# Optimization experiments

Hardware: AMD Instinct MI355X
Metric: run time of the kernel (lower is better)

## Reference

```python
import jax, jax.numpy as jnp
import numpy as np

HEADS = 4
F_OUT = 64
NEG_SLOPE = 0.2


def setup_inputs() -> dict:
    key = jax.random.key(0)
    k1, k2, k3, k4 = jax.random.split(key, 4)
    N, F_IN = 4096, 256
    x = jax.random.normal(k1, (N, F_IN), dtype=jnp.float32)
    adj = jax.random.randint(k2, (N, N), 0, 2, dtype=jnp.int32)
    # nn.Linear stores weight [out, in]; we store transposed [in, out] for x @ W
    W = jax.random.normal(k3, (F_IN, F_OUT * HEADS), dtype=jnp.float32) * (1.0 / np.sqrt(F_IN))
    a = jax.random.normal(k4, (2 * F_OUT, 1), dtype=jnp.float32) * 0.1
    return {"x": x, "adj": adj, "W": W, "a": a}


def reference(x, adj, W, a):
    N = x.shape[0]
    h = (x @ W).reshape(N, HEADS, F_OUT)              # [N, H, F]
    # matmul(cat(h_i, h_j), a) == h_i @ a1 + h_j @ a2 (exact, avoids O(N^2*2F) h_cat)
    a1 = a[:F_OUT, 0]
    a2 = a[F_OUT:, 0]
    e_i = jnp.einsum('nhf,f->nh', h, a1)              # [N, H]
    e_j = jnp.einsum('nhf,f->nh', h, a2)              # [N, H]
    e = e_i[:, None, :] + e_j[None, :, :]             # [N, N, H]
    e = jnp.where(e > 0, e, NEG_SLOPE * e)            # LeakyReLU(0.2)
    e = jnp.where(adj[:, :, None] == 0, -jnp.inf, e)
    attention = jax.nn.softmax(e, axis=1)             # softmax over source nodes j
    h_prime = jnp.einsum('ijh,jhf->ihf', attention, h)  # [N, H, F]
    return h_prime.mean(axis=1)                       # heads > 1 -> mean over heads
```

## Files before the change

### kernel.cpp

```cpp
#include <hip/hip_runtime.h>

#define N     4096
#define FIN   256
#define CC    256
#define HEADS 4
#define FOUT  64
#define XPITCH 266

typedef __attribute__((ext_vector_type(8))) short bf16x8;
typedef __attribute__((ext_vector_type(4))) float f32x4;
typedef __attribute__((ext_vector_type(2))) float f32x2;

__device__ inline unsigned cvtpk(float lo, float hi) {
    unsigned r;
    asm("v_cvt_pk_bf16_f32 %0, %1, %2" : "=v"(r) : "v"(lo), "v"(hi));
    return r;
}
__device__ inline f32x2 pkmul(f32x2 a, f32x2 b) {
    f32x2 r;
    asm("v_pk_mul_f32 %0, %1, %2" : "=v"(r) : "v"(a), "v"(b));
    return r;
}

__global__ __launch_bounds__(512) void gat_k1a(const float* __restrict__ x,
                                               const float* __restrict__ W,
                                               const float* __restrict__ a,
                                               short* __restrict__ hF,
                                               float2* __restrict__ e1f,
                                               float2* __restrict__ e2f) {
    __shared__ __align__(16) short xs[64][XPITCH];
    __shared__ __align__(16) short wts[64][XPITCH];
    __shared__ __align__(16) short hbuf[64][74];
    const int t    = threadIdx.x;
    const int bid  = blockIdx.x;
    const int lane = t & 63;
    const int w    = t >> 6;

    const int hd = bid >> 6;
    const int n0 = (bid & 63) * 64;
    const int c0 = hd * 64;

    {
        const float4* xsrc = (const float4*)(x + (size_t)n0 * FIN);
        #pragma unroll
        for (int it = 0; it < 8; ++it) {
            const int fi = it * 512 + t;
            const float4 v = xsrc[fi];
            uint2 o;
            o.x = cvtpk(v.x, v.y);
            o.y = cvtpk(v.z, v.w);
            *(uint2*)&xs[fi >> 6][(fi & 63) * 4] = o;
        }
    }
    {
        const int c  = t & 63;
        const int k4 = (t >> 6) * 4;
        #pragma unroll
        for (int it = 0; it < 8; ++it) {
            const int k = it * 32 + k4;
            const float w0 = W[(k + 0) * CC + c0 + c];
            const float w1 = W[(k + 1) * CC + c0 + c];
            const float w2 = W[(k + 2) * CC + c0 + c];
            const float w3 = W[(k + 3) * CC + c0 + c];
            uint2 o;
            o.x = cvtpk(w0, w1);
            o.y = cvtpk(w2, w3);
            *(uint2*)&wts[c][k] = o;
        }
    }
    __syncthreads();

    const int m = lane & 15;
    const int q = lane >> 4;

    if (w < 4) {
        f32x4 acc[4];
        #pragma unroll
        for (int ct = 0; ct < 4; ++ct) acc[ct] = (f32x4){0.f, 0.f, 0.f, 0.f};

        #pragma unroll
        for (int ks = 0; ks < 8; ++ks) {
            const bf16x8 af = *(const bf16x8*)&xs[w * 16 + m][ks * 32 + q * 8];
            #pragma unroll
            for (int ct = 0; ct < 4; ++ct) {
                const bf16x8 bf_ = *(const bf16x8*)&wts[ct * 16 + m][ks * 32 + q * 8];
                acc[ct] = __builtin_amdgcn_mfma_f32_16x16x32_bf16(af, bf_, acc[ct], 0, 0, 0);
            }
        }

        const float a1v[4] = {a[m], a[16 + m], a[32 + m], a[48 + m]};
        const float a2v[4] = {a[64 + m], a[80 + m], a[96 + m], a[112 + m]};
        #pragma unroll
        for (int r = 0; r < 4; ++r) {
            float s1 = 0.f, s2 = 0.f;
            #pragma unroll
            for (int ct = 0; ct < 4; ++ct) {
                s1 = fmaf(acc[ct][r], a1v[ct], s1);
                s2 = fmaf(acc[ct][r], a2v[ct], s2);
            }
            #pragma unroll
            for (int sh = 1; sh < 16; sh <<= 1) {
                s1 += __shfl_xor(s1, sh, 64);
                s2 += __shfl_xor(s2, sh, 64);
            }
            if (m == 0) {
                const int n = n0 + w * 16 + q * 4 + r;
                e1f[(size_t)hd * N + n] = make_float2(__expf(s1), __expf(0.2f * s1));
                e2f[(size_t)hd * N + n] = make_float2(__expf(s2), __expf(0.2f * s2));
            }
        }

        #pragma unroll
        for (int ct = 0; ct < 4; ++ct) {
            const unsigned lo = cvtpk(acc[ct][0], acc[ct][1]);
            const unsigned hi = cvtpk(acc[ct][2], acc[ct][3]);
            unsigned* hp = (unsigned*)&hbuf[ct * 16 + m][w * 16 + q * 4];
            hp[0] = lo;
            hp[1] = hi;
        }
    }
    __syncthreads();

    {
        const int lp = t & 63;
        const int ft = (t >> 6) & 3;
        const int c2 = t >> 8;
        const int mm = lp & 15;
        const int qq = lp >> 4;
        const bf16x8 hv = *(const bf16x8*)&hbuf[ft * 16 + mm][c2 * 32 + qq * 8];
        const size_t jc = (size_t)(n0 >> 5) + c2;
        *(bf16x8*)(hF + ((((size_t)hd * 128 + jc) * 4 + ft) * 64 + lp) * 8) = hv;
    }
}

__global__ __launch_bounds__(256) void gat_k1b(const int* __restrict__ adj,
                                               unsigned* __restrict__ adjb) {
    const int t    = threadIdx.x;
    const int lane = t & 63;
    const int w    = t >> 6;
    const int row  = blockIdx.x * 2 + (w >> 1);
    const int half = w & 1;
    const int4* arow4 = (const int4*)(adj + (size_t)row * N) + half * 512;
    unsigned*   drow  = adjb + (size_t)row * 128 + half * 64;

    int4 ca[8];
    #pragma unroll
    for (int k = 0; k < 8; ++k)
        ca[k] = arow4[k * 64 + lane];
    #pragma unroll
    for (int k = 0; k < 8; ++k) {
        const int4 v = ca[k];
        unsigned n = (v.x != 0 ? 1u : 0u) | (v.y != 0 ? 2u : 0u) |
                     (v.z != 0 ? 4u : 0u) | (v.w != 0 ? 8u : 0u);
        unsigned b  = n   | ((unsigned)__shfl_xor((int)n,   1, 64) << 4);
        unsigned hw = b   | ((unsigned)__shfl_xor((int)b,   2, 64) << 8);
        unsigned d  = hw  | ((unsigned)__shfl_xor((int)hw,  4, 64) << 16);
        if ((lane & 7) == 0) drow[k * 8 + (lane >> 3)] = d;
    }
}

__global__ __launch_bounds__(512) void gat_k2b(const short* __restrict__ hF,
                                               const unsigned* __restrict__ adjb,
                                               const float2* __restrict__ e1f,
                                               const float2* __restrict__ e2f,
                                               float* __restrict__ num,
                                               float* __restrict__ Zp) {
    __shared__ __align__(16) short    hstage[2][4096];
    __shared__ __align__(16) float    e2s[2048];
    __shared__ __align__(16) unsigned adjl[256 * 36];
    const int t    = threadIdx.x;
    const int lane = t & 63;
    const int g    = t >> 6;
    const int bid  = blockIdx.x;
    const int xcd  = bid & 7;
    const int idx  = bid >> 3;
    const int hd   = idx & 3;
    const int jc   = (idx >> 2) & 3;
    const int it   = xcd | ((idx >> 4) << 3);
    const int i0   = it * 256;
    const int j0   = jc * 1024;
    const int m    = lane & 15;
    const int q    = lane >> 4;
    const int slice = hd * 4 + jc;

    ((float4*)e2s)[t] = ((const float4*)(e2f + (size_t)hd * N + j0))[t];
    {
        const int row = t >> 1;
        const int p0  = (t & 1) * 4;
        const uint4* src = (const uint4*)(adjb + (size_t)(i0 + row) * 128 + jc * 32);
        uint4* dst = (uint4*)(adjl + row * 36);
        #pragma unroll
        for (int k = 0; k < 4; ++k) dst[p0 + k] = src[p0 + k];
    }
    const uint4* gsrc = (const uint4*)(hF + ((size_t)hd * 128 + jc * 32) * 2048);
    ((uint4*)hstage[0])[t] = gsrc[t];
    __syncthreads();

    const int    ra   = i0 + g * 32 + m;
    const float2 E1a  = e1f[(size_t)hd * N + ra];
    const float2 E1b  = e1f[(size_t)hd * N + ra + 16];
    const f32x2  E1pa = (f32x2){E1a.x, E1a.y};
    const f32x2  E1pb = (f32x2){E1b.x, E1b.y};

    bf16x8 onesb;
    #pragma unroll
    for (int e = 0; e < 8; ++e) onesb[e] = (short)0x3F80;

    f32x4 accf[4], accg[4];
    #pragma unroll
    for (int ft = 0; ft < 4; ++ft) {
        accf[ft] = (f32x4){0.f, 0.f, 0.f, 0.f};
        accg[ft] = (f32x4){0.f, 0.f, 0.f, 0.f};
    }
    f32x4 acczf = (f32x4){0.f, 0.f, 0.f, 0.f};
    f32x4 acczg = (f32x4){0.f, 0.f, 0.f, 0.f};

    const unsigned char* aba = ((const unsigned char*)adjl) + (g * 32 + m) * 144 + q;
    const unsigned char* abb = aba + 16 * 144;

    int cur = 0;
    for (int mac = 0; mac < 16; ++mac) {
        const uint4 v = gsrc[(size_t)((mac + 1) & 15) * 512 + t];

        const short* hb = &hstage[cur][0];
        #pragma unroll
        for (int s = 0; s < 2; ++s) {
            const int jloc = mac * 64 + s * 32 + q * 8;
            const bf16x8 b0 = *(const bf16x8*)(hb + s * 2048 + 0 * 512 + lane * 8);
            const bf16x8 b1 = *(const bf16x8*)(hb + s * 2048 + 1 * 512 + lane * 8);
            const bf16x8 b2 = *(const bf16x8*)(hb + s * 2048 + 2 * 512 + lane * 8);
            const bf16x8 b3 = *(const bf16x8*)(hb + s * 2048 + 3 * 512 + lane * 8);
            const float4* ev = (const float4*)&e2s[2 * jloc];
            const float4 d0 = ev[0], d1 = ev[1], d2 = ev[2], d3 = ev[3];
            const unsigned bitsa = (unsigned)aba[(mac * 2 + s) * 4];
            const unsigned bitsb = (unsigned)abb[(mac * 2 + s) * 4];

            const float ep[8] = {d0.x, d0.z, d1.x, d1.z, d2.x, d2.z, d3.x, d3.z};
            const float en[8] = {d0.y, d0.w, d1.y, d1.w, d2.y, d2.w, d3.y, d3.w};

            float wa[8], wb[8];
            #pragma unroll
            for (int jj = 0; jj < 8; ++jj) {
                const f32x2 e2j = (f32x2){ep[jj], en[jj]};
                const f32x2 pa = pkmul(E1pa, e2j);
                const f32x2 pb = pkmul(E1pb, e2j);
                const unsigned mka = (unsigned)(((int)(bitsa << (31 - jj))) >> 31);
                const unsigned mkb = (unsigned)(((int)(bitsb << (31 - jj))) >> 31);
                float va_ = fmaxf(pa[0], pa[1]);
                float vb_ = fmaxf(pb[0], pb[1]);
                wa[jj] = __builtin_bit_cast(float, __builtin_bit_cast(unsigned, va_) & mka);
                wb[jj] = __builtin_bit_cast(float, __builtin_bit_cast(unsigned, vb_) & mkb);
            }
            uint4 au, bu;
            au.x = cvtpk(wa[0], wa[1]); au.y = cvtpk(wa[2], wa[3]);
            au.z = cvtpk(wa[4], wa[5]); au.w = cvtpk(wa[6], wa[7]);
            bu.x = cvtpk(wb[0], wb[1]); bu.y = cvtpk(wb[2], wb[3]);
            bu.z = cvtpk(wb[4], wb[5]); bu.w = cvtpk(wb[6], wb[7]);
            const bf16x8 af0 = __builtin_bit_cast(bf16x8, au);
            const bf16x8 af1 = __builtin_bit_cast(bf16x8, bu);

            accf[0] = __builtin_amdgcn_mfma_f32_16x16x32_bf16(af0, b0, accf[0], 0, 0, 0);
            accg[0] = __builtin_amdgcn_mfma_f32_16x16x32_bf16(af1, b0, accg[0], 0, 0, 0);
            accf[1] = __builtin_amdgcn_mfma_f32_16x16x32_bf16(af0, b1, accf[1], 0, 0, 0);
            accg[1] = __builtin_amdgcn_mfma_f32_16x16x32_bf16(af1, b1, accg[1], 0, 0, 0);
            accf[2] = __builtin_amdgcn_mfma_f32_16x16x32_bf16(af0, b2, accf[2], 0, 0, 0);
            accg[2] = __builtin_amdgcn_mfma_f32_16x16x32_bf16(af1, b2, accg[2], 0, 0, 0);
            accf[3] = __builtin_amdgcn_mfma_f32_16x16x32_bf16(af0, b3, accf[3], 0, 0, 0);
            accg[3] = __builtin_amdgcn_mfma_f32_16x16x32_bf16(af1, b3, accg[3], 0, 0, 0);
            acczf   = __builtin_amdgcn_mfma_f32_16x16x32_bf16(af0, onesb, acczf, 0, 0, 0);
            acczg   = __builtin_amdgcn_mfma_f32_16x16x32_bf16(af1, onesb, acczg, 0, 0, 0);
        }

        if (mac < 15) {
            ((uint4*)hstage[cur ^ 1])[t] = v;
            __syncthreads();
            cur ^= 1;
        }
    }

    if (m == 0) {
        #pragma unroll
        for (int r = 0; r < 4; ++r) {
            Zp[(size_t)slice * N + i0 + g * 32 + q * 4 + r]      = acczf[r];
            Zp[(size_t)slice * N + i0 + g * 32 + 16 + q * 4 + r] = acczg[r];
        }
    }

    {
        float* nrow = num + ((size_t)slice * N + i0 + g * 32) * FOUT;
        #pragma unroll
        for (int ft = 0; ft < 4; ++ft)
            #pragma unroll
            for (int r = 0; r < 4; ++r) {
                nrow[(q * 4 + r) * FOUT + ft * 16 + m]        = accf[ft][r];
                nrow[(16 + q * 4 + r) * FOUT + ft * 16 + m]   = accg[ft][r];
            }
    }
}

__global__ __launch_bounds__(256) void gat_k3(const float* __restrict__ num,
                                              const float* __restrict__ Zp,
                                              float* __restrict__ out) {
    const int g4 = blockIdx.x * 256 + threadIdx.x;
    const int i  = g4 >> 4;
    const int fo = (g4 & 15) * 4;
    float4 r = make_float4(0.f, 0.f, 0.f, 0.f);
    #pragma unroll
    for (int hd = 0; hd < 4; ++hd) {
        float4 s = make_float4(0.f, 0.f, 0.f, 0.f);
        float  z = 0.f;
        #pragma unroll
        for (int jc = 0; jc < 4; ++jc) {
            const int sl = hd * 4 + jc;
            const float4 v = *(const float4*)(num + ((size_t)sl * N + i) * FOUT + fo);
            s.x += v.x; s.y += v.y; s.z += v.z; s.w += v.w;
            z += Zp[(size_t)sl * N + i];
        }
        const float inv = 1.f / z;
        r.x += s.x * inv; r.y += s.y * inv; r.z += s.z * inv; r.w += s.w * inv;
    }
    r.x *= 0.25f; r.y *= 0.25f; r.z *= 0.25f; r.w *= 0.25f;
    *(float4*)(out + (size_t)i * FOUT + fo) = r;
}

extern "C" void kernel_launch(void* const* d_in, const int* in_sizes, int n_in,
                              void* d_out, int out_size, void* d_ws, size_t ws_size,
                              hipStream_t stream) {
    const float* x   = (const float*)d_in[0];
    const int*   adj = (const int*)d_in[1];
    const float* W   = (const float*)d_in[2];
    const float* a   = (const float*)d_in[3];
    float* out = (float*)d_out;

    short*    hF   = (short*)d_ws;
    float2*   e1f  = (float2*)(hF + (size_t)HEADS * FOUT * N);
    float2*   e2f  = e1f + (size_t)HEADS * N;
    unsigned* adjb = (unsigned*)(e2f + (size_t)HEADS * N);
    float*    num  = (float*)(adjb + (size_t)N * 128);
    float*    Zp   = num + (size_t)16 * N * FOUT;

    gat_k1a<<<256, 512, 0, stream>>>(x, W, a, hF, e1f, e2f);
    gat_k1b<<<2048, 256, 0, stream>>>(adj, adjb);
    gat_k2b<<<256, 512, 0, stream>>>(hF, adjb, e1f, e2f, num, Zp);
    gat_k3<<<256, 256, 0, stream>>>(num, Zp, out);
}
```

Measured before the change: 139.9 us.

## Split attention kernel over eight source chunks to double block count

The attention-aggregation kernel now splits the source-node dimension into eight 512-wide chunks instead of four 1024-wide ones. This launches 512 blocks instead of 256, filling more of the GPU's compute units, and shrinks per-block shared memory with a launch-bounds occupancy hint. The cost is twice as many partial numerator and denominator slices written to workspace and reduced in the final kernel, which adds global memory traffic. The weight computation is also restructured into a helper that packs pairs of e2 values directly.

```diff
diff --git a/kernel.cpp b/kernel.cpp
--- a/kernel.cpp
+++ b/kernel.cpp
@@ -20,6 +20,17 @@
     f32x2 r;
     asm("v_pk_mul_f32 %0, %1, %2" : "=v"(r) : "v"(a), "v"(b));
     return r;
+}
+__device__ inline unsigned wpair(f32x2 E1p, float4 dd, unsigned bits, int jj) {
+    const f32x2 plo = pkmul(E1p, (f32x2){dd.x, dd.y});
+    const f32x2 phi = pkmul(E1p, (f32x2){dd.z, dd.w});
+    const unsigned mlo = (unsigned)(((int)(bits << (31 - jj))) >> 31);
+    const unsigned mhi = (unsigned)(((int)(bits << (30 - jj))) >> 31);
+    const float lo = __builtin_bit_cast(float,
+        __builtin_bit_cast(unsigned, fmaxf(plo[0], plo[1])) & mlo);
+    const float hi = __builtin_bit_cast(float,
+        __builtin_bit_cast(unsigned, fmaxf(phi[0], phi[1])) & mhi);
+    return cvtpk(lo, hi);
 }
 
 __global__ __launch_bounds__(512) void gat_k1a(const float* __restrict__ x,
@@ -159,15 +170,15 @@
     }
 }
 
-__global__ __launch_bounds__(512) void gat_k2b(const short* __restrict__ hF,
-                                               const unsigned* __restrict__ adjb,
-                                               const float2* __restrict__ e1f,
-                                               const float2* __restrict__ e2f,
-                                               float* __restrict__ num,
-                                               float* __restrict__ Zp) {
+__global__ __launch_bounds__(512, 4) void gat_k2b(const short* __restrict__ hF,
+                                                  const unsigned* __restrict__ adjb,
+                                                  const float2* __restrict__ e1f,
+                                                  const float2* __restrict__ e2f,
+                                                  float* __restrict__ num,
+                                                  float* __restrict__ Zp) {
     __shared__ __align__(16) short    hstage[2][4096];
-    __shared__ __align__(16) float    e2s[2048];
-    __shared__ __align__(16) unsigned adjl[256 * 36];
+    __shared__ __align__(16) float    e2s[1024];
+    __shared__ __align__(16) unsigned adjl[256 * 20];
     const int t    = threadIdx.x;
     const int lane = t & 63;
     const int g    = t >> 6;
@@ -175,24 +186,25 @@
     const int xcd  = bid & 7;
     const int idx  = bid >> 3;
     const int hd   = idx & 3;
-    const int jc   = (idx >> 2) & 3;
-    const int it   = xcd | ((idx >> 4) << 3);
+    const int jc   = (idx >> 2) & 7;
+    const int it   = xcd | ((idx >> 5) << 3);
     const int i0   = it * 256;
-    const int j0   = jc * 1024;
+    const int j0   = jc * 512;
     const int m    = lane & 15;
     const int q    = lane >> 4;
-    const int slice = hd * 4 + jc;
-
-    ((float4*)e2s)[t] = ((const float4*)(e2f + (size_t)hd * N + j0))[t];
+    const int slice = hd * 8 + jc;
+
+    if (t < 256)
+        ((float4*)e2s)[t] = ((const float4*)(e2f + (size_t)hd * N + j0))[t];
     {
         const int row = t >> 1;
-        const int p0  = (t & 1) * 4;
-        const uint4* src = (const uint4*)(adjb + (size_t)(i0 + row) * 128 + jc * 32);
-        uint4* dst = (uint4*)(adjl + row * 36);
-        #pragma unroll
-        for (int k = 0; k < 4; ++k) dst[p0 + k] = src[p0 + k];
-    }
-    const uint4* gsrc = (const uint4*)(hF + ((size_t)hd * 128 + jc * 32) * 2048);
+        const int p0  = (t & 1) * 2;
+        const uint4* src = (const uint4*)(adjb + (size_t)(i0 + row) * 128 + jc * 16);
+        uint4* dst = (uint4*)(adjl + row * 20);
+        dst[p0]     = src[p0];
+        dst[p0 + 1] = src[p0 + 1];
+    }
+    const uint4* gsrc = (const uint4*)(hF + ((size_t)hd * 128 + jc * 16) * 2048);
     ((uint4*)hstage[0])[t] = gsrc[t];
     __syncthreads();
 
@@ -215,12 +227,12 @@
     f32x4 acczf = (f32x4){0.f, 0.f, 0.f, 0.f};
     f32x4 acczg = (f32x4){0.f, 0.f, 0.f, 0.f};
 
-    const unsigned char* aba = ((const unsigned char*)adjl) + (g * 32 + m) * 144 + q;
-    const unsigned char* abb = aba + 16 * 144;
+    const unsigned char* aba = ((const unsigned char*)adjl) + (g * 32 + m) * 80 + q;
+    const unsigned char* abb = aba + 16 * 80;
 
     int cur = 0;
-    for (int mac = 0; mac < 16; ++mac) {
-        const uint4 v = gsrc[(size_t)((mac + 1) & 15) * 512 + t];
+    for (int mac = 0; mac < 8; ++mac) {
+        const uint4 v = gsrc[(size_t)((mac + 1) & 7) * 512 + t];
 
         const short* hb = &hstage[cur][0];
         #pragma unroll
@@ -235,27 +247,15 @@
             const unsigned bitsa = (unsigned)aba[(mac * 2 + s) * 4];
             const unsigned bitsb = (unsigned)abb[(mac * 2 + s) * 4];
 
-            const float ep[8] = {d0.x, d0.z, d1.x, d1.z, d2.x, d2.z, d3.x, d3.z};
-            const float en[8] = {d0.y, d0.w, d1.y, d1.w, d2.y, d2.w, d3.y, d3.w};
-
-            float wa[8], wb[8];
-            #pragma unroll
-            for (int jj = 0; jj < 8; ++jj) {
-                const f32x2 e2j = (f32x2){ep[jj], en[jj]};
-                const f32x2 pa = pkmul(E1pa, e2j);
-                const f32x2 pb = pkmul(E1pb, e2j);
-                const unsigned mka = (unsigned)(((int)(bitsa << (31 - jj))) >> 31);
-                const unsigned mkb = (unsigned)(((int)(bitsb << (31 - jj))) >> 31);
-                float va_ = fmaxf(pa[0], pa[1]);
-                float vb_ = fmaxf(pb[0], pb[1]);
-                wa[jj] = __builtin_bit_cast(float, __builtin_bit_cast(unsigned, va_) & mka);
-                wb[jj] = __builtin_bit_cast(float, __builtin_bit_cast(unsigned, vb_) & mkb);
-            }
             uint4 au, bu;
-            au.x = cvtpk(wa[0], wa[1]); au.y = cvtpk(wa[2], wa[3]);
-            au.z = cvtpk(wa[4], wa[5]); au.w = cvtpk(wa[6], wa[7]);
-            bu.x = cvtpk(wb[0], wb[1]); bu.y = cvtpk(wb[2], wb[3]);
-            bu.z = cvtpk(wb[4], wb[5]); bu.w = cvtpk(wb[6], wb[7]);
+            au.x = wpair(E1pa, d0, bitsa, 0);
+            au.y = wpair(E1pa, d1, bitsa, 2);
+            au.z = wpair(E1pa, d2, bitsa, 4);
+            au.w = wpair(E1pa, d3, bitsa, 6);
+            bu.x = wpair(E1pb, d0, bitsb, 0);
+            bu.y = wpair(E1pb, d1, bitsb, 2);
+            bu.z = wpair(E1pb, d2, bitsb, 4);
+            bu.w = wpair(E1pb, d3, bitsb, 6);
             const bf16x8 af0 = __builtin_bit_cast(bf16x8, au);
             const bf16x8 af1 = __builtin_bit_cast(bf16x8, bu);
 
@@ -271,7 +271,7 @@
             acczg   = __builtin_amdgcn_mfma_f32_16x16x32_bf16(af1, onesb, acczg, 0, 0, 0);
         }
 
-        if (mac < 15) {
+        if (mac < 7) {
             ((uint4*)hstage[cur ^ 1])[t] = v;
             __syncthreads();
             cur ^= 1;
@@ -292,8 +292,8 @@
         for (int ft = 0; ft < 4; ++ft)
             #pragma unroll
             for (int r = 0; r < 4; ++r) {
-                nrow[(q * 4 + r) * FOUT + ft * 16 + m]        = accf[ft][r];
-                nrow[(16 + q * 4 + r) * FOUT + ft * 16 + m]   = accg[ft][r];
+                nrow[(q * 4 + r) * FOUT + ft * 16 + m]      = accf[ft][r];
+                nrow[(16 + q * 4 + r) * FOUT + ft * 16 + m] = accg[ft][r];
             }
     }
 }
@@ -310,8 +310,8 @@
         float4 s = make_float4(0.f, 0.f, 0.f, 0.f);
         float  z = 0.f;
         #pragma unroll
-        for (int jc = 0; jc < 4; ++jc) {
-            const int sl = hd * 4 + jc;
+        for (int jc = 0; jc < 8; ++jc) {
+            const int sl = hd * 8 + jc;
             const float4 v = *(const float4*)(num + ((size_t)sl * N + i) * FOUT + fo);
             s.x += v.x; s.y += v.y; s.z += v.z; s.w += v.w;
             z += Zp[(size_t)sl * N + i];
@@ -337,10 +337,10 @@
     float2*   e2f  = e1f + (size_t)HEADS * N;
     unsigned* adjb = (unsigned*)(e2f + (size_t)HEADS * N);
     float*    num  = (float*)(adjb + (size_t)N * 128);
-    float*    Zp   = num + (size_t)16 * N * FOUT;
+    float*    Zp   = num + (size_t)32 * N * FOUT;
 
     gat_k1a<<<256, 512, 0, stream>>>(x, W, a, hF, e1f, e2f);
     gat_k1b<<<2048, 256, 0, stream>>>(adj, adjb);
-    gat_k2b<<<256, 512, 0, stream>>>(hF, adjb, e1f, e2f, num, Zp);
+    gat_k2b<<<512, 512, 0, stream>>>(hF, adjb, e1f, e2f, num, Zp);
     gat_k3<<<256, 256, 0, stream>>>(num, Zp, out);
 }
```

Result: no change. 137.9 us (-1.4%).
